# Performance work log

Hardware: AMD Instinct MI355X
Metric: run time of the kernel (lower is better)

The kernel has to match this reference:

```python
import jax, jax.numpy as jnp
import numpy as np

NEG = -1e4      # BigBird additive mask value
LN_EPS = 1e-12  # BERT-style LayerNorm eps


def _bigbird_forward(xs_pad, mask, Wq, bq, Wk, bk, Wv, bv, Wo, bo, gamma, beta, rand_idx):
    b, n, hsz = xs_pad.shape
    H = rand_idx.shape[0]
    nb = rand_idx.shape[1] + 2          # one rand row per non-edge query block
    BS = n // nb                        # block size
    d = hsz // H
    r = rand_idx.shape[2]
    scale = 1.0 / np.sqrt(d).astype(np.float32)

    mf = mask.reshape(b, n).astype(xs_pad.dtype)   # (b,n) 1=token, 0=pad
    mb = mf.reshape(b, nb, BS)                     # blocked mask

    def proj(W, bias):
        return (xs_pad @ W + bias).reshape(b, n, H, d).transpose(0, 2, 1, 3)

    q = proj(Wq, bq) * scale            # (b,H,n,d)
    k = proj(Wk, bk)
    v = proj(Wv, bv)
    qb = q.reshape(b, H, nb, BS, d)
    kb = k.reshape(b, H, nb, BS, d)
    vb = v.reshape(b, H, nb, BS, d)

    # ---- global rows: first / last query block attend to all keys ----
    def full_row(qi):                   # qi: (b,H,BS,d)
        s = jnp.einsum('bhqd,bhkd->bhqk', qi, k) + (1.0 - mf)[:, None, None, :] * NEG
        return jnp.einsum('bhqk,bhkd->bhqd', jax.nn.softmax(s, axis=-1), v)

    ctx_first = full_row(qb[:, :, 0])
    ctx_last = full_row(qb[:, :, nb - 1])

    # ---- random key/value blocks: per-head, per-query-block gather ----
    hidx = jnp.arange(H)[:, None, None]
    rand_k = kb[:, hidx, rand_idx].reshape(b, H, nb - 2, r * BS, d)
    rand_v = vb[:, hidx, rand_idx].reshape(b, H, nb - 2, r * BS, d)
    rand_m = mb[:, rand_idx].reshape(b, H, nb - 2, r * BS)

    def sparse_row(qi, kc, vc, mc):     # kc:(b,H,K,d), mc:(b,H,K)
        s = jnp.einsum('bhqd,bhkd->bhqk', qi, kc) + (1.0 - mc)[:, :, None, :] * NEG
        return jnp.einsum('bhqk,bhkd->bhqd', jax.nn.softmax(s, axis=-1), vc)

    def gather_blocks(ids, ridx):
        kc = jnp.concatenate([kb[:, :, j] for j in ids] + [rand_k[:, :, ridx]], axis=2)
        vc = jnp.concatenate([vb[:, :, j] for j in ids] + [rand_v[:, :, ridx]], axis=2)
        mc = jnp.concatenate([jnp.broadcast_to(mb[:, None, j], (b, H, BS)) for j in ids]
                             + [rand_m[:, :, ridx]], axis=2)
        return kc, vc, mc

    # second / penultimate query blocks: window + globals + rand
    ctx_second = sparse_row(qb[:, :, 1], *gather_blocks([0, 1, 2, nb - 1], 0))
    ctx_penult = sparse_row(qb[:, :, nb - 2], *gather_blocks([nb - 3, nb - 2, nb - 1, 0], nb - 3))

    # ---- middle rows i in [2, nb-3]: 3-block sliding window + first/last global + r random ----
    nmid = nb - 4
    mid = jnp.arange(2, nb - 2)
    win = mid[:, None] + jnp.arange(-1, 2)[None, :]        # (nmid,3)
    k_win = kb[:, :, win].reshape(b, H, nmid, 3 * BS, d)
    v_win = vb[:, :, win].reshape(b, H, nmid, 3 * BS, d)
    m_win = jnp.broadcast_to(mb[:, win].reshape(b, 1, nmid, 3 * BS), (b, H, nmid, 3 * BS))

    def rep_glob(t):                     # (b,H,BS,...) -> (b,H,nmid,BS,...)
        return jnp.broadcast_to(t[:, :, None], (b, H, nmid) + t.shape[2:])

    k_mid = jnp.concatenate([k_win, rep_glob(kb[:, :, 0]), rep_glob(kb[:, :, nb - 1]),
                             rand_k[:, :, 1:nb - 3]], axis=3)
    v_mid = jnp.concatenate([v_win, rep_glob(vb[:, :, 0]), rep_glob(vb[:, :, nb - 1]),
                             rand_v[:, :, 1:nb - 3]], axis=3)
    m_first = jnp.broadcast_to(mb[:, None, None, 0], (b, H, nmid, BS))
    m_last = jnp.broadcast_to(mb[:, None, None, nb - 1], (b, H, nmid, BS))
    m_mid = jnp.concatenate([m_win, m_first, m_last, rand_m[:, :, 1:nb - 3]], axis=3)

    s_mid = jnp.einsum('bhmqd,bhmkd->bhmqk', qb[:, :, 2:nb - 2], k_mid) \
            + (1.0 - m_mid)[:, :, :, None, :] * NEG
    ctx_mid = jnp.einsum('bhmqk,bhmkd->bhmqd', jax.nn.softmax(s_mid, axis=-1), v_mid)

    ctx = jnp.concatenate([ctx_first[:, :, None], ctx_second[:, :, None], ctx_mid,
                           ctx_penult[:, :, None], ctx_last[:, :, None]], axis=2)
    ctx = ctx.reshape(b, H, n, d).transpose(0, 2, 1, 3).reshape(b, n, hsz)
    ctx = ctx * mf[:, :, None]           # from_mask on output rows

    # BigBirdSelfOutput: dense + residual + LayerNorm (dropout=0 / eval)
    y = ctx @ Wo + bo + xs_pad
    mu = y.mean(-1, keepdims=True)
    var = ((y - mu) ** 2).mean(-1, keepdims=True)
    return (y - mu) * jax.lax.rsqrt(var + LN_EPS) * gamma + beta


def setup_inputs() -> dict:
    key = jax.random.key(0)
    ks = jax.random.split(key, 6)
    B, N, HSZ, H, BS, R = 4, 4096, 1024, 16, 64, 3
    NB = N // BS
    init = lambda k, shp: jax.random.normal(k, shp, dtype=jnp.float32) * 0.02
    return {
        'xs_pad': jax.random.normal(ks[0], (B, N, HSZ), dtype=jnp.float32),
        'mask': jnp.ones((B, 1, N), dtype=jnp.int32),
        'Wq': init(ks[1], (HSZ, HSZ)), 'bq': jnp.zeros((HSZ,), jnp.float32),
        'Wk': init(ks[2], (HSZ, HSZ)), 'bk': jnp.zeros((HSZ,), jnp.float32),
        'Wv': init(ks[3], (HSZ, HSZ)), 'bv': jnp.zeros((HSZ,), jnp.float32),
        'Wo': init(ks[4], (HSZ, HSZ)), 'bo': jnp.zeros((HSZ,), jnp.float32),
        'gamma': jnp.ones((HSZ,), jnp.float32), 'beta': jnp.zeros((HSZ,), jnp.float32),
        'rand_idx': jax.random.randint(ks[5], (H, NB - 2, R), 1, NB - 1).astype(jnp.int32),
    }


def reference(xs_pad, mask, Wq, bq, Wk, bk, Wv, bv, Wo, bo, gamma, beta, rand_idx):
    return _bigbird_forward(xs_pad, mask, Wq, bq, Wk, bk, Wv, bv, Wo, bo, gamma, beta, rand_idx)
```

## Files before the change

### kernel.cpp

```cpp
#include <hip/hip_runtime.h>
#include <hip/hip_bf16.h>

#define B_   4
#define N_   4096
#define HSZ  1024
#define H_   16
#define D_   64
#define NB_  64
#define R_   3
#define M_   (B_*N_)
#define NEGV (-1e4f)
#define LOG2E 1.4426950408889634f

typedef float f32x4 __attribute__((ext_vector_type(4)));
typedef short s16x8 __attribute__((ext_vector_type(8)));
typedef __bf16 b16x8 __attribute__((ext_vector_type(8)));

__device__ __forceinline__ f32x4 mfma16(s16x8 a, s16x8 b, f32x4 c) {
  return __builtin_amdgcn_mfma_f32_16x16x32_bf16(
      __builtin_bit_cast(b16x8, a), __builtin_bit_cast(b16x8, b), c, 0, 0, 0);
}

__device__ __forceinline__ short f2b(float x) {
  __hip_bfloat16 h = __float2bfloat16(x);
  return (short)__builtin_bit_cast(unsigned short, h);
}

__device__ __forceinline__ unsigned pack2(float a, float b) {
  return (unsigned)(unsigned short)f2b(a) |
         ((unsigned)(unsigned short)f2b(b) << 16);
}

__device__ __forceinline__ void gl_lds16(const short* g, short* l) {
  __builtin_amdgcn_global_load_lds(
      (const __attribute__((address_space(1))) unsigned int*)g,
      (__attribute__((address_space(3))) unsigned int*)l, 16, 0, 0);
}

__global__ __launch_bounds__(256) void k_conv(const float* __restrict__ in,
                                              short* __restrict__ out) {
  size_t i = ((size_t)blockIdx.x * 256 + threadIdx.x) * 8;
  float4 a = *(const float4*)&in[i];
  float4 b = *(const float4*)&in[i + 4];
  s16x8 o;
  o[0] = f2b(a.x); o[1] = f2b(a.y); o[2] = f2b(a.z); o[3] = f2b(a.w);
  o[4] = f2b(b.x); o[5] = f2b(b.y); o[6] = f2b(b.z); o[7] = f2b(b.w);
  *(s16x8*)&out[i] = o;
}

__global__ __launch_bounds__(256) void k_wt(const float* __restrict__ Wq,
                                            const float* __restrict__ Wk,
                                            const float* __restrict__ Wv,
                                            const float* __restrict__ Wo,
                                            short* __restrict__ out) {
  const int z = blockIdx.z;
  const float* src = (z == 0) ? Wq : (z == 1) ? Wk : (z == 2) ? Wv : Wo;
  short* dst = out + (size_t)z * HSZ * HSZ;
  __shared__ __align__(16) float t[64][68];
  const int tk = blockIdx.x * 64, tn = blockIdx.y * 64;
  const int tid = threadIdx.x;
#pragma unroll
  for (int r = 0; r < 4; ++r) {
    int c = tid + r * 256;
    int row = c >> 4, seg = c & 15;
    *(float4*)&t[row][seg * 4] =
        *(const float4*)&src[(size_t)(tk + row) * HSZ + tn + seg * 4];
  }
  __syncthreads();
#pragma unroll
  for (int r = 0; r < 2; ++r) {
    int c = tid + r * 256;
    int row = c >> 3, seg = c & 7;
    s16x8 o;
#pragma unroll
    for (int u = 0; u < 8; ++u) o[u] = f2b(t[seg * 8 + u][row]);
    *(s16x8*)&dst[(size_t)(tn + row) * HSZ + tk + seg * 8] = o;
  }
}

__global__ __launch_bounds__(256) void k_attb(const int* __restrict__ mask,
                                              float* __restrict__ attb) {
  int i = blockIdx.x * 256 + threadIdx.x;
  attb[i] = (1.0f - (float)mask[i]) * NEGV * LOG2E;
}

template <int PATH>
__global__ __launch_bounds__(256) void k_gemm(
    const short* __restrict__ A, const short* __restrict__ WT,
    const float* __restrict__ bias0, const float* __restrict__ bias1,
    short* __restrict__ o0, short* __restrict__ o1,
    const float* __restrict__ xs, float* __restrict__ yout) {
  const int z = (PATH == 0) ? blockIdx.z : 0;
  const int wsel = (PATH == 0) ? z : (PATH == 1 ? 2 : 3);
  const short* Bt = WT + (size_t)wsel * HSZ * HSZ;
  const float* bias = (PATH == 0 && z == 1) ? bias1 : bias0;
  short* outb = (PATH == 0 && z == 1) ? o1 : o0;
  const float alpha = (PATH == 0 && z == 0) ? 0.125f * LOG2E : 1.0f;

  __shared__ __align__(16) short a_lds[128][64];
  __shared__ __align__(16) short b_lds[128][64];

  const int tid = threadIdx.x, lane = tid & 63, wave = tid >> 6;
  const int lq = lane & 15, g = lane >> 4;
  const int wm = (wave & 1) * 64, wn = (wave >> 1) * 64;
  const int tm = blockIdx.x * 128, tn = blockIdx.y * 128;

  const int srow = wave * 32 + (lane >> 3);
  const int scol = ((lane & 7) ^ ((lane >> 3) & 7)) * 8;

  f32x4 acc[4][4] = {};

  for (int kt = 0; kt < HSZ; kt += 64) {
    __syncthreads();
#pragma unroll
    for (int u = 0; u < 4; ++u) {
      gl_lds16(&A[(size_t)(tm + srow + u * 8) * HSZ + kt + scol],
               &a_lds[wave * 32 + u * 8][0]);
      gl_lds16(&Bt[(size_t)(tn + srow + u * 8) * HSZ + kt + scol],
               &b_lds[wave * 32 + u * 8][0]);
    }
    __syncthreads();
    const int sw = (lq & 7) << 3;
#pragma unroll
    for (int kk = 0; kk < 2; ++kk) {
      const int ko = (kk * 32 + g * 8) ^ sw;
      s16x8 af[4], bf[4];
#pragma unroll
      for (int i = 0; i < 4; ++i)
        af[i] = *(const s16x8*)&a_lds[wm + i * 16 + lq][ko];
#pragma unroll
      for (int j = 0; j < 4; ++j)
        bf[j] = *(const s16x8*)&b_lds[wn + j * 16 + lq][ko];
#pragma unroll
      for (int i = 0; i < 4; ++i)
#pragma unroll
        for (int j = 0; j < 4; ++j)
          acc[i][j] = (PATH == 1) ? mfma16(af[i], bf[j], acc[i][j])
                                  : mfma16(bf[j], af[i], acc[i][j]);
    }
  }

  if (PATH == 1) {
#pragma unroll
    for (int j = 0; j < 4; ++j) {
      const int col = tn + wn + j * 16 + lq;
      const int hh = col >> 6, dd = col & 63;
      const float bi = bias[col];
#pragma unroll
      for (int i = 0; i < 4; ++i) {
        const int nrow = tm + wm + i * 16 + g * 4;
        const int bb = nrow >> 12, nn = nrow & (N_ - 1);
        uint2 w;
        w.x = pack2(acc[i][j][0] + bi, acc[i][j][1] + bi);
        w.y = pack2(acc[i][j][2] + bi, acc[i][j][3] + bi);
        *(uint2*)&o0[(((size_t)bb * H_ + hh) * D_ + dd) * N_ + nn] = w;
      }
    }
    return;
  }

#pragma unroll
  for (int i = 0; i < 4; ++i) {
    const int row = tm + wm + i * 16 + lq;
#pragma unroll
    for (int j = 0; j < 4; ++j) {
      const int colb = tn + wn + j * 16 + g * 4;
      const float4 bi = *(const float4*)&bias[colb];
      if (PATH == 0) {
        const int bb = row >> 12, nn = row & (N_ - 1);
        const int hh = colb >> 6, dd = colb & 63;
        uint2 w;
        w.x = pack2((acc[i][j][0] + bi.x) * alpha,
                    (acc[i][j][1] + bi.y) * alpha);
        w.y = pack2((acc[i][j][2] + bi.z) * alpha,
                    (acc[i][j][3] + bi.w) * alpha);
        *(uint2*)&outb[(((size_t)bb * H_ + hh) * N_ + nn) * D_ + dd] = w;
      } else {
        const size_t idx = (size_t)row * HSZ + colb;
        const float4 xv = *(const float4*)&xs[idx];
        float4 yv;
        yv.x = acc[i][j][0] + bi.x + xv.x;
        yv.y = acc[i][j][1] + bi.y + xv.y;
        yv.z = acc[i][j][2] + bi.z + xv.z;
        yv.w = acc[i][j][3] + bi.w + xv.w;
        *(float4*)&yout[idx] = yv;
      }
    }
  }
}

__global__ __launch_bounds__(256) void k_attn(
    const short* __restrict__ Q, const short* __restrict__ K,
    const short* __restrict__ VT, const float* __restrict__ attb,
    const int* __restrict__ mask, const int* __restrict__ rnd,
    short* __restrict__ ctx, float* __restrict__ pO,
    float* __restrict__ pm, float* __restrict__ pl) {
  const int s = blockIdx.x, h = blockIdx.y, b = blockIdx.z;
  const int tid = threadIdx.x, lane = tid & 63, wave = tid >> 6;
  const int g = lane >> 4, lq = lane & 15;

  __shared__ __align__(16) short k_lds[64][72];
  __shared__ __align__(16) short vt_lds[64][72];
  __shared__ __align__(16) short p_lds[4][16][72];
  __shared__ __align__(16) float bias_s[64];
  __shared__ int list_s[8];
  __shared__ int Ls;

  const bool mid = (s < 62);
  const int qb = mid ? (s + 1) : (((s - 62) >> 3) ? (NB_ - 1) : 0);

  if (tid == 0) {
    int L;
    if (!mid) {
      int chunk = (s - 62) & 7;
#pragma unroll
      for (int i = 0; i < 8; ++i) list_s[i] = chunk * 8 + i;
      L = 8;
    } else {
      const int* rp = rnd + ((size_t)h * (NB_ - 2) + (qb - 1)) * R_;
      int n;
      if (qb == 1) {
        list_s[0] = 0; list_s[1] = 1; list_s[2] = 2; list_s[3] = NB_ - 1; n = 4;
      } else if (qb == NB_ - 2) {
        list_s[0] = NB_ - 3; list_s[1] = NB_ - 2; list_s[2] = NB_ - 1;
        list_s[3] = 0; n = 4;
      } else {
        list_s[0] = qb - 1; list_s[1] = qb; list_s[2] = qb + 1;
        list_s[3] = 0; list_s[4] = NB_ - 1; n = 5;
      }
      for (int j = 0; j < R_; ++j) list_s[n + j] = rp[j];
      L = n + R_;
    }
    Ls = L;
  }

  const size_t bh = (size_t)b * H_ + h;
  const size_t qrow = bh * N_ + (size_t)qb * 64 + wave * 16 + lq;
  s16x8 qf0 = *(const s16x8*)&Q[qrow * D_ + g * 8];
  s16x8 qf1 = *(const s16x8*)&Q[qrow * D_ + 32 + g * 8];

  __syncthreads();
  const int L = Ls;

  const int r0 = tid >> 3, sg0 = tid & 7;
  const int r1 = 32 + (tid >> 3), sg1 = tid & 7;

  s16x8 kr0, kr1, vr0, vr1;
  float br = 0.0f;
  {
    const int kb = list_s[0];
    const short* kp = &K[(bh * N_ + (size_t)kb * 64) * D_];
    const short* vp = &VT[bh * (size_t)D_ * N_ + (size_t)kb * 64];
    kr0 = *(const s16x8*)&kp[r0 * D_ + sg0 * 8];
    kr1 = *(const s16x8*)&kp[r1 * D_ + sg1 * 8];
    vr0 = *(const s16x8*)&vp[(size_t)r0 * N_ + sg0 * 8];
    vr1 = *(const s16x8*)&vp[(size_t)r1 * N_ + sg1 * 8];
    if (tid < 64) br = attb[(size_t)b * N_ + kb * 64 + tid];
  }

  f32x4 o[4] = {};
  float m_run = -INFINITY, ssum = 0.0f;

  for (int it = 0; it < L; ++it) {
    *(s16x8*)&k_lds[r0][sg0 * 8] = kr0;
    *(s16x8*)&k_lds[r1][sg1 * 8] = kr1;
    *(s16x8*)&vt_lds[r0][sg0 * 8] = vr0;
    *(s16x8*)&vt_lds[r1][sg1 * 8] = vr1;
    if (tid < 64) bias_s[tid] = br;
    if (it + 1 < L) {
      const int kb = list_s[it + 1];
      const short* kp = &K[(bh * N_ + (size_t)kb * 64) * D_];
      const short* vp = &VT[bh * (size_t)D_ * N_ + (size_t)kb * 64];
      kr0 = *(const s16x8*)&kp[r0 * D_ + sg0 * 8];
      kr1 = *(const s16x8*)&kp[r1 * D_ + sg1 * 8];
      vr0 = *(const s16x8*)&vp[(size_t)r0 * N_ + sg0 * 8];
      vr1 = *(const s16x8*)&vp[(size_t)r1 * N_ + sg1 * 8];
      if (tid < 64) br = attb[(size_t)b * N_ + kb * 64 + tid];
    }
    __syncthreads();

    f32x4 st[4];
#pragma unroll
    for (int f = 0; f < 4; ++f) {
      f32x4 acc0 = {};
#pragma unroll
      for (int kk = 0; kk < 2; ++kk) {
        s16x8 af = *(const s16x8*)&k_lds[f * 16 + lq][kk * 32 + g * 8];
        acc0 = mfma16(af, kk ? qf1 : qf0, acc0);
      }
      f32x4 b4 = *(const f32x4*)&bias_s[f * 16 + g * 4];
      st[f] = acc0 + b4;
    }

    float t0 = fmaxf(fmaxf(st[0][0], st[0][1]), fmaxf(st[0][2], st[0][3]));
    float t1 = fmaxf(fmaxf(st[1][0], st[1][1]), fmaxf(st[1][2], st[1][3]));
    float t2 = fmaxf(fmaxf(st[2][0], st[2][1]), fmaxf(st[2][2], st[2][3]));
    float t3 = fmaxf(fmaxf(st[3][0], st[3][1]), fmaxf(st[3][2], st[3][3]));
    float bm = fmaxf(fmaxf(t0, t1), fmaxf(t2, t3));
    bm = fmaxf(bm, __shfl_xor(bm, 16));
    bm = fmaxf(bm, __shfl_xor(bm, 32));
    if (!__all(bm <= m_run + 8.0f)) {
      float mnew = fmaxf(m_run, bm);
      float al = exp2f(m_run - mnew);
      f32x4 av;
      av[0] = __shfl(al, g * 4 + 0);
      av[1] = __shfl(al, g * 4 + 1);
      av[2] = __shfl(al, g * 4 + 2);
      av[3] = __shfl(al, g * 4 + 3);
#pragma unroll
      for (int j = 0; j < 4; ++j) o[j] *= av;
      ssum *= al;
      m_run = mnew;
    }
    float psum = 0.0f;
#pragma unroll
    for (int f = 0; f < 4; ++f)
#pragma unroll
      for (int e = 0; e < 4; ++e) {
        float p = exp2f(st[f][e] - m_run);
        st[f][e] = p;
        psum += p;
      }
    psum += __shfl_xor(psum, 16);
    psum += __shfl_xor(psum, 32);
    ssum += psum;

#pragma unroll
    for (int f = 0; f < 4; ++f) {
      uint2 w = make_uint2(pack2(st[f][0], st[f][1]),
                           pack2(st[f][2], st[f][3]));
      *(uint2*)&p_lds[wave][lq][f * 16 + g * 4] = w;
    }

#pragma unroll
    for (int kk = 0; kk < 2; ++kk) {
      s16x8 pa = *(const s16x8*)&p_lds[wave][lq][kk * 32 + g * 8];
#pragma unroll
      for (int j = 0; j < 4; ++j) {
        s16x8 bv = *(const s16x8*)&vt_lds[j * 16 + lq][kk * 32 + g * 8];
        o[j] = mfma16(pa, bv, o[j]);
      }
    }
    __syncthreads();
  }

  if (mid) {
    float rs = (float)mask[(size_t)b * N_ + qb * 64 + wave * 16 + lq] / ssum;
    float s0 = __shfl(rs, g * 4 + 0);
    float s1 = __shfl(rs, g * 4 + 1);
    float s2 = __shfl(rs, g * 4 + 2);
    float s3 = __shfl(rs, g * 4 + 3);
#pragma unroll
    for (int j = 0; j < 4; ++j) {
      k_lds[wave * 16 + g * 4 + 0][j * 16 + lq] = f2b(o[j][0] * s0);
      k_lds[wave * 16 + g * 4 + 1][j * 16 + lq] = f2b(o[j][1] * s1);
      k_lds[wave * 16 + g * 4 + 2][j * 16 + lq] = f2b(o[j][2] * s2);
      k_lds[wave * 16 + g * 4 + 3][j * 16 + lq] = f2b(o[j][3] * s3);
    }
    __syncthreads();
#pragma unroll
    for (int p = 0; p < 2; ++p) {
      int c = tid + p * 256;
      int row = c >> 3, seg = c & 7;
      *(s16x8*)&ctx[((size_t)b * N_ + qb * 64 + row) * HSZ + h * D_ + seg * 8] =
          *(const s16x8*)&k_lds[row][seg * 8];
    }
  } else {
    const int e2 = s - 62;
    const int qsel = e2 >> 3, chunk = e2 & 7;
    const size_t eidx = (bh * 2 + qsel) * 8 + chunk;
    float* po = pO + eidx * 4096;
#pragma unroll
    for (int j = 0; j < 4; ++j)
#pragma unroll
      for (int e = 0; e < 4; ++e)
        po[(wave * 16 + g * 4 + e) * 64 + j * 16 + lq] = o[j][e];
    if (lane < 16) {
      pm[eidx * 64 + wave * 16 + lane] = m_run;
      pl[eidx * 64 + wave * 16 + lane] = ssum;
    }
  }
}

__global__ __launch_bounds__(256) void k_comb(
    const float* __restrict__ pO, const float* __restrict__ pm,
    const float* __restrict__ pl, const int* __restrict__ mask,
    short* __restrict__ ctx) {
  const int qsel = blockIdx.x, h = blockIdx.y, b = blockIdx.z;
  const int qb = qsel ? NB_ - 1 : 0;
  const int tid = threadIdx.x;
  const int q = tid >> 2, dq = tid & 3;
  const size_t base = (((size_t)b * H_ + h) * 2 + qsel) * 8;

  float mv[8];
  float M = -INFINITY;
#pragma unroll
  for (int i = 0; i < 8; ++i) {
    mv[i] = pm[(base + i) * 64 + q];
    M = fmaxf(M, mv[i]);
  }
  float Lsum = 0.0f;
#pragma unroll
  for (int i = 0; i < 8; ++i) {
    float w = exp2f(mv[i] - M);
    mv[i] = w;
    Lsum += pl[(base + i) * 64 + q] * w;
  }
  f32x4 acc[4] = {};
#pragma unroll
  for (int i = 0; i < 8; ++i) {
    const float* p = pO + (base + i) * 4096 + q * 64 + dq * 16;
    float w = mv[i];
#pragma unroll
    for (int u = 0; u < 4; ++u) {
      f32x4 v = *(const f32x4*)&p[u * 4];
      acc[u] += v * w;
    }
  }
  float sc = (float)mask[(size_t)b * N_ + qb * 64 + q] / Lsum;
  s16x8 out0, out1;
#pragma unroll
  for (int u = 0; u < 8; ++u) {
    out0[u] = f2b(acc[u >> 2][u & 3] * sc);
    out1[u] = f2b(acc[2 + (u >> 2)][u & 3] * sc);
  }
  short* dst = &ctx[((size_t)b * N_ + qb * 64 + q) * HSZ + h * D_ + dq * 16];
  *(s16x8*)dst = out0;
  *(s16x8*)(dst + 8) = out1;
}

__global__ __launch_bounds__(256) void k_ln(float* __restrict__ y,
                                            const float* __restrict__ gamma,
                                            const float* __restrict__ beta) {
  const int row = blockIdx.x, tid = threadIdx.x, lane = tid & 63,
            wave = tid >> 6;
  __shared__ float s_sum[4], s_sq[4];
  float4 v = *(const float4*)&y[(size_t)row * HSZ + tid * 4];
  float s = v.x + v.y + v.z + v.w;
  float q = v.x * v.x + v.y * v.y + v.z * v.z + v.w * v.w;
#pragma unroll
  for (int m = 1; m <= 32; m <<= 1) {
    s += __shfl_xor(s, m);
    q += __shfl_xor(q, m);
  }
  if (lane == 0) { s_sum[wave] = s; s_sq[wave] = q; }
  __syncthreads();
  float S = s_sum[0] + s_sum[1] + s_sum[2] + s_sum[3];
  float Qs = s_sq[0] + s_sq[1] + s_sq[2] + s_sq[3];
  float mu = S * (1.0f / HSZ);
  float var = Qs * (1.0f / HSZ) - mu * mu;
  float r = rsqrtf(var + 1e-12f);
  float4 g = *(const float4*)&gamma[tid * 4];
  float4 be = *(const float4*)&beta[tid * 4];
  float4 outv;
  outv.x = (v.x - mu) * r * g.x + be.x;
  outv.y = (v.y - mu) * r * g.y + be.y;
  outv.z = (v.z - mu) * r * g.z + be.z;
  outv.w = (v.w - mu) * r * g.w + be.w;
  *(float4*)&y[(size_t)row * HSZ + tid * 4] = outv;
}

extern "C" void kernel_launch(void* const* d_in, const int* in_sizes, int n_in,
                              void* d_out, int out_size, void* d_ws,
                              size_t ws_size, hipStream_t stream) {
  const float* xs = (const float*)d_in[0];
  const int* mask = (const int*)d_in[1];
  const float* Wq = (const float*)d_in[2];
  const float* bq = (const float*)d_in[3];
  const float* Wk = (const float*)d_in[4];
  const float* bk = (const float*)d_in[5];
  const float* Wv = (const float*)d_in[6];
  const float* bv = (const float*)d_in[7];
  const float* Wo = (const float*)d_in[8];
  const float* bo = (const float*)d_in[9];
  const float* gamma = (const float*)d_in[10];
  const float* beta = (const float*)d_in[11];
  const int* rnd = (const int*)d_in[12];
  float* yout = (float*)d_out;

  char* ws = (char*)d_ws;
  const size_t SZ_XS = (size_t)M_ * HSZ * 2;
  const size_t SZ_WT = (size_t)4 * HSZ * HSZ * 2;
  short* xsb = (short*)ws;
  short* wt = (short*)(ws + SZ_XS);
  short* qbuf = (short*)(ws + SZ_XS + SZ_WT);
  short* kbuf = qbuf + (size_t)M_ * HSZ;
  short* vtb = kbuf + (size_t)M_ * HSZ;
  char* after = ws + SZ_XS + SZ_WT + 3 * SZ_XS;
  float* attb = (float*)after;
  float* pO = (float*)(after + (1 << 20));
  float* pm = pO + (size_t)1024 * 4096;
  float* pl = pm + (size_t)1024 * 64;

  k_conv<<<8192, 256, 0, stream>>>(xs, xsb);
  k_wt<<<dim3(16, 16, 4), 256, 0, stream>>>(Wq, Wk, Wv, Wo, wt);
  k_attb<<<64, 256, 0, stream>>>(mask, attb);
  k_gemm<0><<<dim3(128, 8, 2), 256, 0, stream>>>(
      xsb, wt, bq, bk, qbuf, kbuf, nullptr, nullptr);
  k_gemm<1><<<dim3(128, 8, 1), 256, 0, stream>>>(
      xsb, wt, bv, nullptr, vtb, nullptr, nullptr, nullptr);
  k_attn<<<dim3(78, H_, B_), 256, 0, stream>>>(qbuf, kbuf, vtb, attb, mask,
                                               rnd, xsb, pO, pm, pl);
  k_comb<<<dim3(2, H_, B_), 256, 0, stream>>>(pO, pm, pl, mask, xsb);
  k_gemm<2><<<dim3(128, 8, 1), 256, 0, stream>>>(
      xsb, wt, bo, nullptr, nullptr, nullptr, xs, yout);
  k_ln<<<M_, 256, 0, stream>>>(yout, gamma, beta);
}
```

Baseline: 382.8 us.

## Double-buffer GEMM LDS tiles and fold mask bias into attention kernel

The GEMM main loop now uses two LDS buffers and issues global-to-LDS loads for tile k+2 while computing on tile k, using vmcnt waits and raw barriers instead of the load-sync-compute pattern. This aims to hide global load latency behind MFMA work in all three GEMMs. It doubles LDS usage to 64KB per block, which may lower occupancy. Separately, the tiny k_attb launch is removed and the mask bias is computed inline in the attention kernel, saving one launch.

```diff
diff --git a/kernel.cpp b/kernel.cpp
--- a/kernel.cpp
+++ b/kernel.cpp
@@ -76,12 +76,6 @@
     for (int u = 0; u < 8; ++u) o[u] = f2b(t[seg * 8 + u][row]);
     *(s16x8*)&dst[(size_t)(tn + row) * HSZ + tk + seg * 8] = o;
   }
-}
-
-__global__ __launch_bounds__(256) void k_attb(const int* __restrict__ mask,
-                                              float* __restrict__ attb) {
-  int i = blockIdx.x * 256 + threadIdx.x;
-  attb[i] = (1.0f - (float)mask[i]) * NEGV * LOG2E;
 }
 
 template <int PATH>
@@ -97,8 +91,8 @@
   short* outb = (PATH == 0 && z == 1) ? o1 : o0;
   const float alpha = (PATH == 0 && z == 0) ? 0.125f * LOG2E : 1.0f;
 
-  __shared__ __align__(16) short a_lds[128][64];
-  __shared__ __align__(16) short b_lds[128][64];
+  __shared__ __align__(16) short a_lds[2][128][64];
+  __shared__ __align__(16) short b_lds[2][128][64];
 
   const int tid = threadIdx.x, lane = tid & 63, wave = tid >> 6;
   const int lq = lane & 15, g = lane >> 4;
@@ -110,27 +104,28 @@
 
   f32x4 acc[4][4] = {};
 
-  for (int kt = 0; kt < HSZ; kt += 64) {
-    __syncthreads();
+  auto STAGE = [&](int buf, int kt) {
 #pragma unroll
     for (int u = 0; u < 4; ++u) {
       gl_lds16(&A[(size_t)(tm + srow + u * 8) * HSZ + kt + scol],
-               &a_lds[wave * 32 + u * 8][0]);
+               &a_lds[buf][wave * 32 + u * 8][0]);
       gl_lds16(&Bt[(size_t)(tn + srow + u * 8) * HSZ + kt + scol],
-               &b_lds[wave * 32 + u * 8][0]);
-    }
-    __syncthreads();
-    const int sw = (lq & 7) << 3;
+               &b_lds[buf][wave * 32 + u * 8][0]);
+    }
+  };
+
+  const int sw = (lq & 7) << 3;
+  auto COMPUTE = [&](int buf) {
 #pragma unroll
     for (int kk = 0; kk < 2; ++kk) {
       const int ko = (kk * 32 + g * 8) ^ sw;
       s16x8 af[4], bf[4];
 #pragma unroll
       for (int i = 0; i < 4; ++i)
-        af[i] = *(const s16x8*)&a_lds[wm + i * 16 + lq][ko];
+        af[i] = *(const s16x8*)&a_lds[buf][wm + i * 16 + lq][ko];
 #pragma unroll
       for (int j = 0; j < 4; ++j)
-        bf[j] = *(const s16x8*)&b_lds[wn + j * 16 + lq][ko];
+        bf[j] = *(const s16x8*)&b_lds[buf][wn + j * 16 + lq][ko];
 #pragma unroll
       for (int i = 0; i < 4; ++i)
 #pragma unroll
@@ -138,7 +133,26 @@
           acc[i][j] = (PATH == 1) ? mfma16(af[i], bf[j], acc[i][j])
                                   : mfma16(bf[j], af[i], acc[i][j]);
     }
-  }
+  };
+
+  STAGE(0, 0);
+  STAGE(1, 64);
+  int cur = 0;
+  for (int s = 0; s < 14; ++s) {
+    asm volatile("s_waitcnt vmcnt(8)" ::: "memory");
+    __builtin_amdgcn_s_barrier();
+    COMPUTE(cur);
+    __builtin_amdgcn_s_barrier();
+    STAGE(cur, (s + 2) * 64);
+    cur ^= 1;
+  }
+  asm volatile("s_waitcnt vmcnt(8)" ::: "memory");
+  __builtin_amdgcn_s_barrier();
+  COMPUTE(cur);
+  cur ^= 1;
+  asm volatile("s_waitcnt vmcnt(0)" ::: "memory");
+  __builtin_amdgcn_s_barrier();
+  COMPUTE(cur);
 
   if (PATH == 1) {
 #pragma unroll
@@ -191,10 +205,9 @@
 
 __global__ __launch_bounds__(256) void k_attn(
     const short* __restrict__ Q, const short* __restrict__ K,
-    const short* __restrict__ VT, const float* __restrict__ attb,
-    const int* __restrict__ mask, const int* __restrict__ rnd,
-    short* __restrict__ ctx, float* __restrict__ pO,
-    float* __restrict__ pm, float* __restrict__ pl) {
+    const short* __restrict__ VT, const int* __restrict__ mask,
+    const int* __restrict__ rnd, short* __restrict__ ctx,
+    float* __restrict__ pO, float* __restrict__ pm, float* __restrict__ pl) {
   const int s = blockIdx.x, h = blockIdx.y, b = blockIdx.z;
   const int tid = threadIdx.x, lane = tid & 63, wave = tid >> 6;
   const int g = lane >> 4, lq = lane & 15;
@@ -255,7 +268,9 @@
     kr1 = *(const s16x8*)&kp[r1 * D_ + sg1 * 8];
     vr0 = *(const s16x8*)&vp[(size_t)r0 * N_ + sg0 * 8];
     vr1 = *(const s16x8*)&vp[(size_t)r1 * N_ + sg1 * 8];
-    if (tid < 64) br = attb[(size_t)b * N_ + kb * 64 + tid];
+    if (tid < 64)
+      br = (1.0f - (float)mask[(size_t)b * N_ + kb * 64 + tid]) *
+           (NEGV * LOG2E);
   }
 
   f32x4 o[4] = {};
@@ -275,7 +290,9 @@
       kr1 = *(const s16x8*)&kp[r1 * D_ + sg1 * 8];
       vr0 = *(const s16x8*)&vp[(size_t)r0 * N_ + sg0 * 8];
       vr1 = *(const s16x8*)&vp[(size_t)r1 * N_ + sg1 * 8];
-      if (tid < 64) br = attb[(size_t)b * N_ + kb * 64 + tid];
+      if (tid < 64)
+        br = (1.0f - (float)mask[(size_t)b * N_ + kb * 64 + tid]) *
+             (NEGV * LOG2E);
     }
     __syncthreads();
 
@@ -487,20 +504,18 @@
   short* kbuf = qbuf + (size_t)M_ * HSZ;
   short* vtb = kbuf + (size_t)M_ * HSZ;
   char* after = ws + SZ_XS + SZ_WT + 3 * SZ_XS;
-  float* attb = (float*)after;
   float* pO = (float*)(after + (1 << 20));
   float* pm = pO + (size_t)1024 * 4096;
   float* pl = pm + (size_t)1024 * 64;
 
   k_conv<<<8192, 256, 0, stream>>>(xs, xsb);
   k_wt<<<dim3(16, 16, 4), 256, 0, stream>>>(Wq, Wk, Wv, Wo, wt);
-  k_attb<<<64, 256, 0, stream>>>(mask, attb);
   k_gemm<0><<<dim3(128, 8, 2), 256, 0, stream>>>(
       xsb, wt, bq, bk, qbuf, kbuf, nullptr, nullptr);
   k_gemm<1><<<dim3(128, 8, 1), 256, 0, stream>>>(
       xsb, wt, bv, nullptr, vtb, nullptr, nullptr, nullptr);
-  k_attn<<<dim3(78, H_, B_), 256, 0, stream>>>(qbuf, kbuf, vtb, attb, mask,
-                                               rnd, xsb, pO, pm, pl);
+  k_attn<<<dim3(78, H_, B_), 256, 0, stream>>>(qbuf, kbuf, vtb, mask, rnd,
+                                               xsb, pO, pm, pl);
   k_comb<<<dim3(2, H_, B_), 256, 0, stream>>>(pO, pm, pl, mask, xsb);
   k_gemm<2><<<dim3(128, 8, 1), 256, 0, stream>>>(
       xsb, wt, bo, nullptr, nullptr, nullptr, xs, yout);
```

Result: faster. 365.7 us (-4.5%).
